# Kernel optimization log

Hardware: AMD Instinct MI355X
Metric: run time of the kernel (lower is better)

Reference implementation:

```python
import jax, jax.numpy as jnp
import numpy as np

B, P, G, C = 16, 32768, 32, 81   # batch, priors, gt boxes per image, classes
IOU_THRESH = 0.5                 # matching() is IoU-threshold matching (standard SSD)
HMR = 3                          # hard_mining_ratio
BETA = 1.0                       # SmoothL1 beta


def _make_boxes(key, lead_shape):
    k1, k2 = jax.random.split(key)
    xy = jax.random.uniform(k1, lead_shape + (2,)) * 0.8
    wh = jax.random.uniform(k2, lead_shape + (2,)) * 0.2 + 0.05
    return jnp.concatenate([xy, xy + wh], axis=-1)  # valid x1y1x2y2 in [0,1]


def setup_inputs() -> dict:
    key = jax.random.key(0)
    ks = jax.random.split(key, 5)
    pred_boxes = _make_boxes(ks[0], (B, P))
    gt_boxes = _make_boxes(ks[1], (B, G))
    # guarantee matches exist: first G priors track the gt boxes closely
    noise = jax.random.normal(ks[2], (B, G, 4)) * 0.005
    pred_boxes = pred_boxes.at[:, :G, :].set(gt_boxes + noise)
    pred_confidences = jax.random.normal(ks[3], (B, P, C), dtype=jnp.float32)
    gt_labels = jax.random.randint(ks[4], (B, G), 0, C, dtype=jnp.int32)
    return {"pred_boxes": pred_boxes, "pred_confidences": pred_confidences,
            "gt_boxes": gt_boxes, "gt_labels": gt_labels}


def _iou(a, b):
    # a: [P,4], b: [G,4] in x1y1x2y2 -> [P,G]
    lt = jnp.maximum(a[:, None, :2], b[None, :, :2])
    rb = jnp.minimum(a[:, None, 2:], b[None, :, 2:])
    inter = jnp.prod(jnp.clip(rb - lt, 0.0), axis=-1)
    area_a = jnp.prod(jnp.clip(a[:, 2:] - a[:, :2], 0.0), axis=-1)
    area_b = jnp.prod(jnp.clip(b[:, 2:] - b[:, :2], 0.0), axis=-1)
    union = area_a[:, None] + area_b[None, :] - inter
    return inter / jnp.maximum(union, 1e-9)


def _smooth_l1(pred, gt):
    d = pred - gt
    ad = jnp.abs(d)
    return jnp.where(ad < BETA, 0.5 * d * d / BETA, ad - 0.5 * BETA)


def _per_image(boxes, conf, gboxes, glabels):
    # boxes [P,4], conf [P,C], gboxes [G,4], glabels [G]
    matches = _iou(boxes, gboxes) > IOU_THRESH          # [P,G]
    total = matches.sum()
    logsm = jax.nn.log_softmax(conf, axis=-1)            # [P,C]
    gathered = logsm[:, glabels]                         # [P,G] log p(label_g | prior_i)
    matches_loss = jnp.sum(jnp.where(matches, gathered, 0.0))
    # mean over the 4 coords, summed over matched (prior, gt) pairs
    sl1 = _smooth_l1(boxes[:, None, :], gboxes[None, :, :]).mean(axis=-1)  # [P,G]
    loc_loss = jnp.sum(jnp.where(matches, sl1, 0.0))
    # hard-negative mining over unmatched priors
    row_matched = matches.any(axis=1)                    # [P]
    sm_max = jnp.max(jax.nn.softmax(conf, axis=-1), axis=-1)  # [P], all > 0
    neg = jnp.where(row_matched, -1.0, sm_max)           # matched rows sort last
    neg = jnp.concatenate([neg, jnp.zeros((1,), neg.dtype)])  # source's extra slot (contributes log1p(0)=0)
    sorted_neg = -jnp.sort(-neg)                         # descending
    k = HMR * total
    keep = (jnp.arange(sorted_neg.shape[0]) < k) & (sorted_neg >= 0.0)
    nomatch_loss = jnp.sum(jnp.where(keep, jnp.log1p(sorted_neg), 0.0))
    return matches_loss, nomatch_loss, loc_loss, total


def reference(pred_boxes, pred_confidences, gt_boxes, gt_labels):
    m, n, l, t = jax.vmap(_per_image)(pred_boxes, pred_confidences, gt_boxes, gt_labels)
    conf_loss = -m.sum() + n.sum()
    # faithful to source: final division uses the LAST image's total_matches
    total_last = t[-1].astype(conf_loss.dtype)
    return (conf_loss + l.sum()) / total_last
```

## Files before the change

### kernel.cpp

```cpp
#include <hip/hip_runtime.h>
#include <hip/hip_bf16.h>
#include <math.h>

#define BB 16
#define PP 32768
#define GG 32
#define NC 81
#define BINSHIFT 13
#define NBINS 8192
#define LOWMASK 0x1FFFu
#define BINBASE 0x3B800000u
#define CAND_CAP 2048
#define SENT 0x7FFFFFFFu
#define SM_BLOCKS 2048
#define BLK_PER_IMG 128
#define NEGINF (-3.0e38f)

struct Accs {
  float m[BB]; float l[BB]; float n[BB];
  unsigned tot[BB]; unsigned rowm[BB];
  unsigned tbin[BB]; unsigned rem[BB]; unsigned candcnt[BB];
};

__device__ __forceinline__ int bin_of(unsigned bits) {
  int bin = ((int)bits - (int)BINBASE) >> BINSHIFT;
  return bin < 0 ? 0 : (bin > NBINS - 1 ? NBINS - 1 : bin);
}

__global__ void init_kernel(Accs* __restrict__ acc) {
  const int t = threadIdx.x;
  if (t < BB) {
    acc->m[t] = 0.f; acc->l[t] = 0.f; acc->n[t] = 0.f;
    acc->tot[t] = 0u; acc->rowm[t] = 0u; acc->candcnt[t] = 0u;
  }
}

__global__ __launch_bounds__(256) void main_kernel(
    const float* __restrict__ pred_boxes,
    const float* __restrict__ conf,
    const float* __restrict__ gt_boxes,
    const int*   __restrict__ gt_labels,
    float* __restrict__ neg,
    Accs* __restrict__ acc)
{
  const int tid  = threadIdx.x;
  const int j    = tid & 7;
  const int rsub = tid >> 3;
  const int b    = blockIdx.x / BLK_PER_IMG;
  const int loc  = blockIdx.x % BLK_PER_IMG;
  const int lane = tid & 63;
  const int w    = tid >> 6;

  __shared__ unsigned s_gm[NC + 3];
  __shared__ float pg[4], pl[4];
  __shared__ unsigned pc[4], pr[4];

  if (tid < NC + 3) s_gm[tid] = 0u;
  __syncthreads();
  if (tid < GG) atomicOr(&s_gm[gt_labels[b * GG + tid]], 1u << tid);
  __syncthreads();

  const float4* gtb = ((const float4*)gt_boxes) + b * GG;
  const float4 gA = gtb[j];
  const float4 gB = gtb[j + 8];
  const float4 gC = gtb[j + 16];
  const float4 gD = gtb[j + 24];
  const float abA = fmaxf(gA.z - gA.x, 0.f) * fmaxf(gA.w - gA.y, 0.f);
  const float abB = fmaxf(gB.z - gB.x, 0.f) * fmaxf(gB.w - gB.y, 0.f);
  const float abC = fmaxf(gC.z - gC.x, 0.f) * fmaxf(gC.w - gC.y, 0.f);
  const float abD = fmaxf(gD.z - gD.x, 0.f) * fmaxf(gD.w - gD.y, 0.f);

  const int  h  = rsub & 3;
  const bool j0 = (j == 0), j4 = (j == 4);
  const bool has3 = (j < 5);
  const float mA0 = (j0 && h > 0) ? NEGINF : 0.f;
  const float mA1 = (j0 && h > 1) ? NEGINF : 0.f;
  const float mA2 = (j0 && h > 2) ? NEGINF : 0.f;
  const float mC1 = (j4 && h < 1) ? NEGINF : 0.f;
  const float mC2 = (j4 && h < 2) ? NEGINF : 0.f;
  const float mC3 = (j4 && h < 3) ? NEGINF : 0.f;
  const int dA = 4 * j - h;
  const int dB = 4 * (j + 8) - h;
  const int dC = 4 * (j + 16) - h;

  const float4* cf = (const float4*)conf;

  float t_g = 0.f, t_l = 0.f;
  unsigned t_c = 0u, t_r = 0u;

  #pragma unroll
  for (int k = 0; k < 8; ++k) {
    const int tile = loc + k * BLK_PER_IMG;
    const int row  = b * PP + tile * 32 + rsub;
    const unsigned abase = (81u * (unsigned)row) >> 2;

    const float4 va = cf[abase + j];
    const float4 vb = cf[abase + j + 8];
    float4 vc = va;
    if (has3) vc = cf[abase + j + 16];
    const float4 pb = ((const float4*)pred_boxes)[row];

    const float a0 = va.x + mA0, a1 = va.y + mA1, a2 = va.z + mA2, a3 = va.w;
    float mx = fmaxf(fmaxf(a0, a1), fmaxf(a2, a3));
    float s  = __expf(a0) + __expf(a1) + __expf(a2) + __expf(a3);
    mx = fmaxf(mx, fmaxf(fmaxf(vb.x, vb.y), fmaxf(vb.z, vb.w)));
    s += __expf(vb.x) + __expf(vb.y) + __expf(vb.z) + __expf(vb.w);
    if (has3) {
      const float e0 = vc.x, e1 = vc.y + mC1, e2 = vc.z + mC2, e3 = vc.w + mC3;
      mx = fmaxf(mx, fmaxf(fmaxf(e0, e1), fmaxf(e2, e3)));
      s += __expf(e0) + __expf(e1) + __expf(e2) + __expf(e3);
    }
    mx = fmaxf(mx, __shfl_xor(mx, 1));  s += __shfl_xor(s, 1);
    mx = fmaxf(mx, __shfl_xor(mx, 2));  s += __shfl_xor(s, 2);
    mx = fmaxf(mx, __shfl_xor(mx, 4));  s += __shfl_xor(s, 4);
    const float lse = __logf(s);
    const float smx = __expf(mx - lse);

    const float aa = fmaxf(pb.z - pb.x, 0.f) * fmaxf(pb.w - pb.y, 0.f);
    unsigned msk = 0u;
    float lsum = 0.f;
    #define IOU_ONE(gb, ab, sh)                                             \
    {                                                                       \
      const float ltx = fmaxf(pb.x, gb.x), lty = fmaxf(pb.y, gb.y);         \
      const float rbx = fminf(pb.z, gb.z), rby = fminf(pb.w, gb.w);         \
      const float inter = fmaxf(rbx - ltx, 0.f) * fmaxf(rby - lty, 0.f);    \
      const float uni = aa + ab - inter;                                    \
      const bool mt = inter > 0.5f * fmaxf(uni, 1e-9f);                     \
      msk |= mt ? (1u << (j + sh)) : 0u;                                    \
      const float d0 = pb.x - gb.x, d1 = pb.y - gb.y;                       \
      const float d2 = pb.z - gb.z, d3 = pb.w - gb.w;                       \
      float sl = 0.f, ad;                                                   \
      ad = fabsf(d0); sl += (ad < 1.f) ? 0.5f * d0 * d0 : ad - 0.5f;        \
      ad = fabsf(d1); sl += (ad < 1.f) ? 0.5f * d1 * d1 : ad - 0.5f;        \
      ad = fabsf(d2); sl += (ad < 1.f) ? 0.5f * d2 * d2 : ad - 0.5f;        \
      ad = fabsf(d3); sl += (ad < 1.f) ? 0.5f * d3 * d3 : ad - 0.5f;        \
      lsum += mt ? sl * 0.25f : 0.f;                                        \
    }
    IOU_ONE(gA, abA, 0)
    IOU_ONE(gB, abB, 8)
    IOU_ONE(gC, abC, 16)
    IOU_ONE(gD, abD, 24)
    #undef IOU_ONE

    msk |= __shfl_xor(msk, 1); msk |= __shfl_xor(msk, 2); msk |= __shfl_xor(msk, 4);
    t_l += lsum;

    if (msk != 0u) {
      float gsum = 0.f;
      if (dA >= 0) gsum += va.x * (float)__popc(msk & s_gm[dA]);
      if (dA + 1 >= 0) gsum += va.y * (float)__popc(msk & s_gm[dA + 1]);
      if (dA + 2 >= 0) gsum += va.z * (float)__popc(msk & s_gm[dA + 2]);
      gsum += va.w * (float)__popc(msk & s_gm[dA + 3]);
      gsum += vb.x * (float)__popc(msk & s_gm[dB]);
      gsum += vb.y * (float)__popc(msk & s_gm[dB + 1]);
      gsum += vb.z * (float)__popc(msk & s_gm[dB + 2]);
      gsum += vb.w * (float)__popc(msk & s_gm[dB + 3]);
      if (has3) {
        gsum += vc.x * (float)__popc(msk & s_gm[dC]);
        if (dC + 1 < NC) gsum += vc.y * (float)__popc(msk & s_gm[dC + 1]);
        if (dC + 2 < NC) gsum += vc.z * (float)__popc(msk & s_gm[dC + 2]);
        if (dC + 3 < NC) gsum += vc.w * (float)__popc(msk & s_gm[dC + 3]);
      }
      t_g += gsum;
      if (j == 0) {
        const unsigned cnt = (unsigned)__popc(msk);
        t_g -= (float)cnt * lse;
        t_c += cnt;
        t_r += 1u;
      }
    }

    if (j == 0) neg[row] = (msk != 0u) ? -1.0f : smx;
  }

  t_g += __shfl_xor(t_g, 1);  t_l += __shfl_xor(t_l, 1);  t_c += __shfl_xor(t_c, 1);  t_r += __shfl_xor(t_r, 1);
  t_g += __shfl_xor(t_g, 2);  t_l += __shfl_xor(t_l, 2);  t_c += __shfl_xor(t_c, 2);  t_r += __shfl_xor(t_r, 2);
  t_g += __shfl_xor(t_g, 4);  t_l += __shfl_xor(t_l, 4);  t_c += __shfl_xor(t_c, 4);  t_r += __shfl_xor(t_r, 4);
  t_g += __shfl_xor(t_g, 8);  t_l += __shfl_xor(t_l, 8);  t_c += __shfl_xor(t_c, 8);  t_r += __shfl_xor(t_r, 8);
  t_g += __shfl_xor(t_g, 16); t_l += __shfl_xor(t_l, 16); t_c += __shfl_xor(t_c, 16); t_r += __shfl_xor(t_r, 16);
  t_g += __shfl_xor(t_g, 32); t_l += __shfl_xor(t_l, 32); t_c += __shfl_xor(t_c, 32); t_r += __shfl_xor(t_r, 32);
  if (lane == 0) { pg[w] = t_g; pl[w] = t_l; pc[w] = t_c; pr[w] = t_r; }
  __syncthreads();
  if (tid == 0) {
    const unsigned c2 = pc[0] + pc[1] + pc[2] + pc[3];
    if (c2 > 0u) {
      atomicAdd(&acc->m[b],    pg[0] + pg[1] + pg[2] + pg[3]);
      atomicAdd(&acc->l[b],    pl[0] + pl[1] + pl[2] + pl[3]);
      atomicAdd(&acc->tot[b],  c2);
      atomicAdd(&acc->rowm[b], pr[0] + pr[1] + pr[2] + pr[3]);
    }
  }
}

__global__ __launch_bounds__(256) void thresh_kernel(const float* __restrict__ neg,
                                                     Accs* __restrict__ acc) {
  const int b = blockIdx.x, tid = threadIdx.x;
  __shared__ unsigned hist[NBINS];
  __shared__ unsigned ps[256];
  __shared__ unsigned s_ch, s_cb;

  const unsigned total  = acc->tot[b];
  const unsigned nvalid = PP - acc->rowm[b];
  unsigned K = 3u * total;
  if (K > nvalid) K = nvalid;
  if (K == 0u) {
    if (tid == 0) { acc->tbin[b] = SENT; acc->rem[b] = 0u; }
    return;
  }

  for (int i = tid; i < NBINS; i += 256) hist[i] = 0u;
  __syncthreads();

  const float4* nb = (const float4*)(neg + ((size_t)b << 15));
  for (int i = tid; i < PP / 4; i += 256) {
    const float4 v4 = nb[i];
    const float vv[4] = {v4.x, v4.y, v4.z, v4.w};
    #pragma unroll
    for (int q = 0; q < 4; ++q)
      if (vv[q] >= 0.f) atomicAdd(&hist[bin_of(__float_as_uint(vv[q]))], 1u);
  }
  __syncthreads();

  unsigned loc = 0;
  #pragma unroll
  for (int q = 0; q < NBINS / 256; ++q) loc += hist[tid * (NBINS / 256) + q];
  ps[tid] = loc;
  __syncthreads();
  for (int off = 1; off < 256; off <<= 1) {
    const unsigned v = (tid + off < 256) ? ps[tid + off] : 0u;
    __syncthreads();
    ps[tid] += v;
    __syncthreads();
  }
  {
    const unsigned above = (tid < 255) ? ps[tid + 1] : 0u;
    if (ps[tid] >= K && above < K) { s_ch = (unsigned)tid; s_cb = above; }
  }
  __syncthreads();
  const unsigned ch = s_ch, cb = s_cb;
  const int CH = NBINS / 256;
  if (tid < CH) ps[tid] = hist[ch * CH + tid];
  __syncthreads();
  for (int off = 1; off < CH; off <<= 1) {
    const unsigned v = (tid < CH && tid + off < CH) ? ps[tid + off] : 0u;
    __syncthreads();
    if (tid < CH) ps[tid] += v;
    __syncthreads();
  }
  if (tid < CH) {
    const unsigned above = cb + ((tid < CH - 1) ? ps[tid + 1] : 0u);
    if (above < K && cb + ps[tid] >= K) {
      acc->tbin[b] = ch * (unsigned)CH + (unsigned)tid;
      acc->rem[b]  = K - above;
    }
  }
}

__global__ __launch_bounds__(256) void sum_kernel(const float* __restrict__ neg,
                                                  float* __restrict__ cand,
                                                  Accs* __restrict__ acc) {
  const int b  = blockIdx.x >> 4;
  const int sl = blockIdx.x & 15;
  const unsigned t = acc->tbin[b];
  const float4* nb = (const float4*)(neg + ((size_t)b << 15)) + sl * 512;
  float sum = 0.f;
  #pragma unroll
  for (int it = 0; it < 2; ++it) {
    const float4 v4 = nb[threadIdx.x + it * 256];
    const float vv[4] = {v4.x, v4.y, v4.z, v4.w};
    #pragma unroll
    for (int q = 0; q < 4; ++q) {
      const float v = vv[q];
      if (v >= 0.f) {
        const unsigned bin = (unsigned)bin_of(__float_as_uint(v));
        if (bin > t) {
          sum += log1pf(v);
        } else if (bin == t) {
          const unsigned idx = atomicAdd(&acc->candcnt[b], 1u);
          if (idx < CAND_CAP) cand[(size_t)b * CAND_CAP + idx] = v;
        }
      }
    }
  }
  sum += __shfl_xor(sum, 1);  sum += __shfl_xor(sum, 2);  sum += __shfl_xor(sum, 4);
  sum += __shfl_xor(sum, 8);  sum += __shfl_xor(sum, 16); sum += __shfl_xor(sum, 32);
  if ((threadIdx.x & 63) == 0 && sum != 0.f) atomicAdd(&acc->n[b], sum);
}

__global__ __launch_bounds__(256) void refine_kernel(const float* __restrict__ neg,
                                                     const float* __restrict__ cand,
                                                     Accs* __restrict__ acc) {
  const int b = blockIdx.x, tid = threadIdx.x;
  __shared__ unsigned h2[NBINS];
  __shared__ unsigned ps[256];
  __shared__ unsigned s_thr, s_rem2;
  const unsigned t = acc->tbin[b];
  if (t == SENT) return;
  const unsigned rem = acc->rem[b];
  const unsigned cc  = acc->candcnt[b];
  const bool fb = (cc > CAND_CAP);
  const int n_src = fb ? PP : (int)cc;
  const float* src = fb ? (neg + ((size_t)b << 15)) : (cand + (size_t)b * CAND_CAP);

  for (int i = tid; i < NBINS; i += 256) h2[i] = 0u;
  __syncthreads();
  for (int i = tid; i < n_src; i += 256) {
    const float v = src[i];
    if (fb) {
      if (!(v >= 0.f) || (unsigned)bin_of(__float_as_uint(v)) != t) continue;
    }
    atomicAdd(&h2[__float_as_uint(v) & LOWMASK], 1u);
  }
  __syncthreads();

  unsigned loc = 0;
  #pragma unroll
  for (int q = 0; q < NBINS / 256; ++q) loc += h2[tid * (NBINS / 256) + q];
  ps[tid] = loc;
  __syncthreads();
  for (int off = 1; off < 256; off <<= 1) {
    const unsigned v = (tid + off < 256) ? ps[tid + off] : 0u;
    __syncthreads();
    ps[tid] += v;
    __syncthreads();
  }
  {
    const unsigned above = (tid < 255) ? ps[tid + 1] : 0u;
    if (ps[tid] >= rem && above < rem) {
      unsigned c = above;
      const int CH = NBINS / 256;
      for (int q = CH - 1; q >= 0; --q) {
        const unsigned hb = h2[tid * CH + q];
        if (c + hb >= rem) { s_thr = (unsigned)(tid * CH + q); s_rem2 = rem - c; break; }
        c += hb;
      }
    }
  }
  __syncthreads();
  const unsigned thr = s_thr, rem2 = s_rem2;

  float sum = 0.f;
  for (int i = tid; i < n_src; i += 256) {
    const float v = src[i];
    if (fb) {
      if (!(v >= 0.f) || (unsigned)bin_of(__float_as_uint(v)) != t) continue;
    }
    if ((__float_as_uint(v) & LOWMASK) > thr) sum += log1pf(v);
  }
  sum += __shfl_xor(sum, 1);  sum += __shfl_xor(sum, 2);  sum += __shfl_xor(sum, 4);
  sum += __shfl_xor(sum, 8);  sum += __shfl_xor(sum, 16); sum += __shfl_xor(sum, 32);
  if ((tid & 63) == 0 && sum != 0.f) atomicAdd(&acc->n[b], sum);
  if (tid == 0 && rem2 > 0u) {
    const unsigned tb = BINBASE + (t << BINSHIFT) + thr;
    atomicAdd(&acc->n[b], (float)rem2 * log1pf(__uint_as_float(tb)));
  }
}

__global__ void finish_kernel(const Accs* __restrict__ acc, float* __restrict__ out) {
  if (threadIdx.x == 0) {
    float conf = 0.f, loc = 0.f;
    #pragma unroll
    for (int b = 0; b < BB; ++b) {
      conf += -acc->m[b] + acc->n[b];
      loc  += acc->l[b];
    }
    out[0] = (conf + loc) / (float)acc->tot[BB - 1];
  }
}

extern "C" void kernel_launch(void* const* d_in, const int* in_sizes, int n_in,
                              void* d_out, int out_size, void* d_ws, size_t ws_size,
                              hipStream_t stream) {
  const float* pred_boxes = (const float*)d_in[0];
  const float* conf       = (const float*)d_in[1];
  const float* gt_boxes   = (const float*)d_in[2];
  const int*   gt_labels  = (const int*)d_in[3];
  float* out = (float*)d_out;

  char* ws = (char*)d_ws;
  float* neg  = (float*)ws;
  float* cand = (float*)(ws + (size_t)BB * PP * 4);
  Accs*  acc  = (Accs*)(ws + (size_t)BB * PP * 4 + (size_t)BB * CAND_CAP * 4);

  hipLaunchKernelGGL(init_kernel, dim3(1), dim3(64), 0, stream, acc);
  hipLaunchKernelGGL(main_kernel, dim3(SM_BLOCKS), dim3(256), 0, stream,
                     pred_boxes, conf, gt_boxes, gt_labels, neg, acc);
  hipLaunchKernelGGL(thresh_kernel, dim3(BB), dim3(256), 0, stream, neg, acc);
  hipLaunchKernelGGL(sum_kernel, dim3(BB * 16), dim3(256), 0, stream, neg, cand, acc);
  hipLaunchKernelGGL(refine_kernel, dim3(BB), dim3(256), 0, stream, neg, cand, acc);
  hipLaunchKernelGGL(finish_kernel, dim3(1), dim3(64), 0, stream, acc, out);
}
```

Before: 111.5 us.

## Fuse negative histogram into main kernel and prefetch next confidence tile

Histogram construction for hard-negative thresholding moves out of the 16-block thresh_kernel into main_kernel, which atomically increments a per-image global histogram as each unmatched row's softmax max is produced. thresh_kernel then only copies that histogram into shared memory, avoiding a serial rescan of the neg array by 16 blocks. main_kernel also software-prefetches the next iteration's confidence vectors, keeps gt boxes and areas in shared memory instead of registers, and branches around the SmoothL1 work for unmatched pairs. The cost is global atomic contention on the histogram bins, a larger init kernel that zeroes the 16×8192 histogram, and extra registers for the prefetch.

```diff
diff --git a/kernel.cpp b/kernel.cpp
--- a/kernel.cpp
+++ b/kernel.cpp
@@ -27,11 +27,14 @@
   return bin < 0 ? 0 : (bin > NBINS - 1 ? NBINS - 1 : bin);
 }
 
-__global__ void init_kernel(Accs* __restrict__ acc) {
-  const int t = threadIdx.x;
-  if (t < BB) {
-    acc->m[t] = 0.f; acc->l[t] = 0.f; acc->n[t] = 0.f;
-    acc->tot[t] = 0u; acc->rowm[t] = 0u; acc->candcnt[t] = 0u;
+__global__ __launch_bounds__(256) void init_kernel(unsigned* __restrict__ hist,
+                                                   Accs* __restrict__ acc) {
+  const unsigned idx = blockIdx.x * 256u + threadIdx.x;
+  if (idx < BB * NBINS) {
+    hist[idx] = 0u;
+  } else {
+    const unsigned t = idx - BB * NBINS;
+    if (t < sizeof(Accs) / 4) ((unsigned*)acc)[t] = 0u;
   }
 }
 
@@ -41,6 +44,7 @@
     const float* __restrict__ gt_boxes,
     const int*   __restrict__ gt_labels,
     float* __restrict__ neg,
+    unsigned* __restrict__ hist,
     Accs* __restrict__ acc)
 {
   const int tid  = threadIdx.x;
@@ -52,23 +56,20 @@
   const int w    = tid >> 6;
 
   __shared__ unsigned s_gm[NC + 3];
+  __shared__ float4 s_gt[GG];
+  __shared__ float  s_ab[GG];
   __shared__ float pg[4], pl[4];
   __shared__ unsigned pc[4], pr[4];
 
   if (tid < NC + 3) s_gm[tid] = 0u;
   __syncthreads();
-  if (tid < GG) atomicOr(&s_gm[gt_labels[b * GG + tid]], 1u << tid);
-  __syncthreads();
-
-  const float4* gtb = ((const float4*)gt_boxes) + b * GG;
-  const float4 gA = gtb[j];
-  const float4 gB = gtb[j + 8];
-  const float4 gC = gtb[j + 16];
-  const float4 gD = gtb[j + 24];
-  const float abA = fmaxf(gA.z - gA.x, 0.f) * fmaxf(gA.w - gA.y, 0.f);
-  const float abB = fmaxf(gB.z - gB.x, 0.f) * fmaxf(gB.w - gB.y, 0.f);
-  const float abC = fmaxf(gC.z - gC.x, 0.f) * fmaxf(gC.w - gC.y, 0.f);
-  const float abD = fmaxf(gD.z - gD.x, 0.f) * fmaxf(gD.w - gD.y, 0.f);
+  if (tid < GG) {
+    atomicOr(&s_gm[gt_labels[b * GG + tid]], 1u << tid);
+    const float4 g = ((const float4*)gt_boxes)[b * GG + tid];
+    s_gt[tid] = g;
+    s_ab[tid] = fmaxf(g.z - g.x, 0.f) * fmaxf(g.w - g.y, 0.f);
+  }
+  __syncthreads();
 
   const int  h  = rsub & 3;
   const bool j0 = (j == 0), j4 = (j == 4);
@@ -83,22 +84,29 @@
   const int dB = 4 * (j + 8) - h;
   const int dC = 4 * (j + 16) - h;
 
-  const float4* cf = (const float4*)conf;
+  const float4* cf  = (const float4*)conf;
+  const float4* pbf = (const float4*)pred_boxes;
 
   float t_g = 0.f, t_l = 0.f;
   unsigned t_c = 0u, t_r = 0u;
 
+  int row = b * PP + loc * 32 + rsub;
+  const unsigned ab0 = (81u * (unsigned)row) >> 2;
+  float4 va = cf[ab0 + j];
+  float4 vb = cf[ab0 + j + 8];
+  float4 vc = has3 ? cf[ab0 + j + 16] : va;
+
   #pragma unroll
   for (int k = 0; k < 8; ++k) {
-    const int tile = loc + k * BLK_PER_IMG;
-    const int row  = b * PP + tile * 32 + rsub;
-    const unsigned abase = (81u * (unsigned)row) >> 2;
-
-    const float4 va = cf[abase + j];
-    const float4 vb = cf[abase + j + 8];
-    float4 vc = va;
-    if (has3) vc = cf[abase + j + 16];
-    const float4 pb = ((const float4*)pred_boxes)[row];
+    const float4 pb = pbf[row];
+
+    float4 nva = va, nvb = vb, nvc = vc;
+    if (k < 7) {
+      const unsigned nab = (81u * (unsigned)(row + BLK_PER_IMG * 32)) >> 2;
+      nva = cf[nab + j];
+      nvb = cf[nab + j + 8];
+      if (has3) nvc = cf[nab + j + 16];
+    }
 
     const float a0 = va.x + mA0, a1 = va.y + mA1, a2 = va.z + mA2, a3 = va.w;
     float mx = fmaxf(fmaxf(a0, a1), fmaxf(a2, a3));
@@ -119,31 +127,40 @@
     const float aa = fmaxf(pb.z - pb.x, 0.f) * fmaxf(pb.w - pb.y, 0.f);
     unsigned msk = 0u;
     float lsum = 0.f;
-    #define IOU_ONE(gb, ab, sh)                                             \
-    {                                                                       \
-      const float ltx = fmaxf(pb.x, gb.x), lty = fmaxf(pb.y, gb.y);         \
-      const float rbx = fminf(pb.z, gb.z), rby = fminf(pb.w, gb.w);         \
-      const float inter = fmaxf(rbx - ltx, 0.f) * fmaxf(rby - lty, 0.f);    \
-      const float uni = aa + ab - inter;                                    \
-      const bool mt = inter > 0.5f * fmaxf(uni, 1e-9f);                     \
-      msk |= mt ? (1u << (j + sh)) : 0u;                                    \
-      const float d0 = pb.x - gb.x, d1 = pb.y - gb.y;                       \
-      const float d2 = pb.z - gb.z, d3 = pb.w - gb.w;                       \
-      float sl = 0.f, ad;                                                   \
-      ad = fabsf(d0); sl += (ad < 1.f) ? 0.5f * d0 * d0 : ad - 0.5f;        \
-      ad = fabsf(d1); sl += (ad < 1.f) ? 0.5f * d1 * d1 : ad - 0.5f;        \
-      ad = fabsf(d2); sl += (ad < 1.f) ? 0.5f * d2 * d2 : ad - 0.5f;        \
-      ad = fabsf(d3); sl += (ad < 1.f) ? 0.5f * d3 * d3 : ad - 0.5f;        \
-      lsum += mt ? sl * 0.25f : 0.f;                                        \
-    }
-    IOU_ONE(gA, abA, 0)
-    IOU_ONE(gB, abB, 8)
-    IOU_ONE(gC, abC, 16)
-    IOU_ONE(gD, abD, 24)
-    #undef IOU_ONE
+    #pragma unroll
+    for (int gi = 0; gi < 4; ++gi) {
+      const int g = j + 8 * gi;
+      const float4 gb = s_gt[g];
+      const float  ab = s_ab[g];
+      const float ltx = fmaxf(pb.x, gb.x), lty = fmaxf(pb.y, gb.y);
+      const float rbx = fminf(pb.z, gb.z), rby = fminf(pb.w, gb.w);
+      const float inter = fmaxf(rbx - ltx, 0.f) * fmaxf(rby - lty, 0.f);
+      const float uni = aa + ab - inter;
+      const bool mt = inter > 0.5f * fmaxf(uni, 1e-9f);
+      if (mt) {
+        msk |= (1u << g);
+        const float d0 = pb.x - gb.x, d1 = pb.y - gb.y;
+        const float d2 = pb.z - gb.z, d3 = pb.w - gb.w;
+        float sl = 0.f, ad;
+        ad = fabsf(d0); sl += (ad < 1.f) ? 0.5f * d0 * d0 : ad - 0.5f;
+        ad = fabsf(d1); sl += (ad < 1.f) ? 0.5f * d1 * d1 : ad - 0.5f;
+        ad = fabsf(d2); sl += (ad < 1.f) ? 0.5f * d2 * d2 : ad - 0.5f;
+        ad = fabsf(d3); sl += (ad < 1.f) ? 0.5f * d3 * d3 : ad - 0.5f;
+        lsum += sl * 0.25f;
+      }
+    }
+    t_l += lsum;
 
     msk |= __shfl_xor(msk, 1); msk |= __shfl_xor(msk, 2); msk |= __shfl_xor(msk, 4);
-    t_l += lsum;
+
+    if (j == 0) {
+      if (msk != 0u) {
+        neg[row] = -1.0f;
+      } else {
+        neg[row] = smx;
+        atomicAdd(&hist[((unsigned)b << 13) + (unsigned)bin_of(__float_as_uint(smx))], 1u);
+      }
+    }
 
     if (msk != 0u) {
       float gsum = 0.f;
@@ -170,7 +187,8 @@
       }
     }
 
-    if (j == 0) neg[row] = (msk != 0u) ? -1.0f : smx;
+    va = nva; vb = nvb; vc = nvc;
+    row += BLK_PER_IMG * 32;
   }
 
   t_g += __shfl_xor(t_g, 1);  t_l += __shfl_xor(t_l, 1);  t_c += __shfl_xor(t_c, 1);  t_r += __shfl_xor(t_r, 1);
@@ -192,10 +210,10 @@
   }
 }
 
-__global__ __launch_bounds__(256) void thresh_kernel(const float* __restrict__ neg,
+__global__ __launch_bounds__(256) void thresh_kernel(const unsigned* __restrict__ hist,
                                                      Accs* __restrict__ acc) {
   const int b = blockIdx.x, tid = threadIdx.x;
-  __shared__ unsigned hist[NBINS];
+  __shared__ unsigned lh[NBINS];
   __shared__ unsigned ps[256];
   __shared__ unsigned s_ch, s_cb;
 
@@ -208,22 +226,13 @@
     return;
   }
 
-  for (int i = tid; i < NBINS; i += 256) hist[i] = 0u;
-  __syncthreads();
-
-  const float4* nb = (const float4*)(neg + ((size_t)b << 15));
-  for (int i = tid; i < PP / 4; i += 256) {
-    const float4 v4 = nb[i];
-    const float vv[4] = {v4.x, v4.y, v4.z, v4.w};
-    #pragma unroll
-    for (int q = 0; q < 4; ++q)
-      if (vv[q] >= 0.f) atomicAdd(&hist[bin_of(__float_as_uint(vv[q]))], 1u);
-  }
+  const unsigned* h = hist + ((unsigned)b << 13);
+  for (int i = tid; i < NBINS; i += 256) lh[i] = h[i];
   __syncthreads();
 
   unsigned loc = 0;
   #pragma unroll
-  for (int q = 0; q < NBINS / 256; ++q) loc += hist[tid * (NBINS / 256) + q];
+  for (int q = 0; q < NBINS / 256; ++q) loc += lh[tid * (NBINS / 256) + q];
   ps[tid] = loc;
   __syncthreads();
   for (int off = 1; off < 256; off <<= 1) {
@@ -239,7 +248,7 @@
   __syncthreads();
   const unsigned ch = s_ch, cb = s_cb;
   const int CH = NBINS / 256;
-  if (tid < CH) ps[tid] = hist[ch * CH + tid];
+  if (tid < CH) ps[tid] = lh[ch * CH + tid];
   __syncthreads();
   for (int off = 1; off < CH; off <<= 1) {
     const unsigned v = (tid < CH && tid + off < CH) ? ps[tid + off] : 0u;
@@ -378,14 +387,17 @@
   float* out = (float*)d_out;
 
   char* ws = (char*)d_ws;
-  float* neg  = (float*)ws;
-  float* cand = (float*)(ws + (size_t)BB * PP * 4);
-  Accs*  acc  = (Accs*)(ws + (size_t)BB * PP * 4 + (size_t)BB * CAND_CAP * 4);
-
-  hipLaunchKernelGGL(init_kernel, dim3(1), dim3(64), 0, stream, acc);
+  float*    neg  = (float*)ws;
+  unsigned* hist = (unsigned*)(ws + (size_t)BB * PP * 4);
+  float*    cand = (float*)(ws + (size_t)BB * PP * 4 + (size_t)BB * NBINS * 4);
+  Accs*     acc  = (Accs*)(ws + (size_t)BB * PP * 4 + (size_t)BB * NBINS * 4
+                              + (size_t)BB * CAND_CAP * 4);
+
+  hipLaunchKernelGGL(init_kernel, dim3((BB * NBINS) / 256 + 1), dim3(256), 0, stream,
+                     hist, acc);
   hipLaunchKernelGGL(main_kernel, dim3(SM_BLOCKS), dim3(256), 0, stream,
-                     pred_boxes, conf, gt_boxes, gt_labels, neg, acc);
-  hipLaunchKernelGGL(thresh_kernel, dim3(BB), dim3(256), 0, stream, neg, acc);
+                     pred_boxes, conf, gt_boxes, gt_labels, neg, hist, acc);
+  hipLaunchKernelGGL(thresh_kernel, dim3(BB), dim3(256), 0, stream, hist, acc);
   hipLaunchKernelGGL(sum_kernel, dim3(BB * 16), dim3(256), 0, stream, neg, cand, acc);
   hipLaunchKernelGGL(refine_kernel, dim3(BB), dim3(256), 0, stream, neg, cand, acc);
   hipLaunchKernelGGL(finish_kernel, dim3(1), dim3(64), 0, stream, acc, out);
```

New measurement: 177.9 us. +59.5%, slower.
